# Optimization experiments

Hardware: AMD Instinct MI355X
Metric: run time of the kernel (lower is better)

## Reference

```python
import jax, jax.numpy as jnp
import numpy as np

B, N = 32, 200000          # images, flattened candidates per image (anchors*classes)
NUM_CLASSES = 21           # VOC-style class count for the label-offset trick
CONF_THR = 0.05            # cfg.PRED_CONF_THR
NMS_THR = 0.5              # cfg.PRED_NMS_THR
TOPK = 500                 # cfg.PRED_SELECT_TOPK
KEEP_MAX = 100             # cfg.PRED_NMS_KEEP


def setup_inputs() -> dict:
    key = jax.random.key(0)
    k1, k2, k3, k4 = jax.random.split(key, 4)
    pscores = jax.random.uniform(k1, (B, N), dtype=jnp.float32)
    # well-formed ltrb boxes in [0,1]: right>left, bottom>top
    xy1 = jax.random.uniform(k2, (B, N, 2), dtype=jnp.float32) * 0.8
    wh = jax.random.uniform(k3, (B, N, 2), dtype=jnp.float32) * 0.2 + 0.01
    pboxes = jnp.concatenate([xy1, xy1 + wh], axis=-1)
    plabels = jax.random.randint(k4, (B, N), 0, NUM_CLASSES)
    return {"pscores": pscores, "pboxes": pboxes, "plabels": plabels}


def _box_iou(a, b):
    # a: [K,4], b: [K,4] ltrb -> [K,K] pairwise IoU (torchvision convention)
    lt = jnp.maximum(a[:, None, :2], b[None, :, :2])
    rb = jnp.minimum(a[:, None, 2:], b[None, :, 2:])
    wh = jnp.clip(rb - lt, 0.0)
    inter = wh[..., 0] * wh[..., 1]
    area_a = (a[:, 2] - a[:, 0]) * (a[:, 3] - a[:, 1])
    area_b = (b[:, 2] - b[:, 0]) * (b[:, 3] - b[:, 1])
    return inter / (area_a[:, None] + area_b[None, :] - inter)


def _greedy_nms(iou_mat, valid, thr):
    # candidates are pre-sorted by score descending (lax.top_k output order)
    K = valid.shape[0]
    idxs = jnp.arange(K)

    def body(keep, i):
        suppressed = jnp.any(keep & (iou_mat[i] > thr) & (idxs < i))
        k = valid[i] & (~suppressed)
        return keep.at[i].set(k), None

    keep, _ = jax.lax.scan(body, jnp.zeros((K,), dtype=bool), idxs)
    return keep


def reference(pscores, pboxes, plabels):
    # ---- threshold + top-k pre-selection (mask_pos AND mask_topk) ----
    scores_k, idx = jax.lax.top_k(pscores, TOPK)          # [B,K] sorted desc
    valid = scores_k > CONF_THR                           # equivalent to mask_pos & mask_topk
    bidx = jnp.arange(B)[:, None]
    boxes_k = pboxes[bidx, idx]                           # [B,K,4]
    labels_k = plabels[bidx, idx]                         # [B,K]

    # ---- multi-class NMS via label offset trick (batched_nms) ----
    max_coord = jnp.max(jnp.where(valid[..., None], boxes_k, 0.0), axis=(1, 2))  # [B]
    offsets = labels_k.astype(boxes_k.dtype) * (max_coord[:, None] + 1.0)
    boxes_nms = boxes_k + offsets[..., None]              # [B,K,4]

    iou = jax.vmap(_box_iou)(boxes_nms, boxes_nms)        # [B,K,K]
    keep = jax.vmap(lambda m, v: _greedy_nms(m, v, NMS_THR))(iou, valid)  # [B,K] bool

    # ---- keep[:num_max] per batch ----
    rank = jnp.cumsum(keep.astype(jnp.int32), axis=1)
    keep = keep & (rank <= KEEP_MAX)

    # compact kept entries to front (jnp.argsort is stable -> score order preserved), pad to KEEP_MAX
    order = jnp.argsort(jnp.where(keep, 0, 1), axis=1)[:, :KEEP_MAX]       # [B,KEEP]
    out_valid = jnp.take_along_axis(keep, order, axis=1)                    # [B,KEEP]
    boxes2 = jnp.take_along_axis(boxes_k, order[..., None], axis=1) * out_valid[..., None]
    scores2 = jnp.take_along_axis(scores_k, order, axis=1) * out_valid
    labels2 = jnp.where(out_valid, jnp.take_along_axis(labels_k, order, axis=1), -1)
    ids_batch2 = jnp.where(out_valid, jnp.arange(B)[:, None], -1)
    return ids_batch2, boxes2, labels2, scores2, out_valid
```

## Files before the change

### kernel.cpp

```cpp
#include <hip/hip_runtime.h>
#include <stdint.h>

#pragma clang fp contract(off)

#define BB 32
#define NN 200000
#define N4 50000
#define KK 500
#define KEEPN 100
#define CONF 0.05f
#define NMSTHR 0.5f
#define SLICES 8
#define SLICE_F4 6250
#define LBINS 8192
#define LSHIFT 19
#define LOCAL_CAP 2048
#define OUT_CAP 576
#define TMPCAP 640
#define OK0 0xBF733333u

typedef unsigned long long u64;


__device__ __forceinline__ unsigned int ordkey(float s) {
    unsigned int u = __float_as_uint(s);
    return (u & 0x80000000u) ? ~u : (u | 0x80000000u);
}

__device__ __forceinline__ void wappend(bool pred, u64 key, u64* keys, int* lcnt, int lane) {
    u64 bm = __ballot(pred);
    int pre = __popcll(bm & ((1ULL << lane) - 1ULL));
    int tt  = __popcll(bm);
    int base = 0;
    if (lane == 0 && tt > 0) base = atomicAdd(lcnt, tt);
    base = __shfl(base, 0);
    if (pred) { int pos = base + pre; if (pos < LOCAL_CAP) keys[pos] = key; }
}

__global__ __launch_bounds__(1024) void select_kernel(const float4* __restrict__ ps4,
                                                      u64* __restrict__ cand,
                                                      unsigned int* __restrict__ cnts) {
    __shared__ unsigned int hist[LBINS];
    __shared__ u64 keys[LOCAL_CAP];
    __shared__ unsigned int h[256];
    __shared__ unsigned int wsum[16];
    __shared__ u64 wmin[16], wmax[16];
    __shared__ u64 s_prefix;
    __shared__ unsigned int s_t13, s_region, s_cntgt;
    __shared__ int s_lcnt, s_sc, s_shift0;

    const int b = blockIdx.y, x = blockIdx.x;
    const int tid = threadIdx.x, lane = tid & 63, wv = tid >> 6;
    const float4* p = ps4 + (size_t)b * N4 + (size_t)x * SLICE_F4;
    const int ebase = x * (SLICE_F4 * 4);

    if (tid == 0) s_lcnt = 0;
    __syncthreads();

    for (int i = tid; i < SLICE_F4; i += 1024) {
        float4 v = p[i];
        int n = ebase + (i << 2);
        unsigned int ux = ordkey(v.x), uy = ordkey(v.y);
        unsigned int uz = ordkey(v.z), uw = ordkey(v.w);
        wappend(ux >= OK0, ((u64)ux << 32) | (unsigned int)(~(unsigned int)(n)),     keys, &s_lcnt, lane);
        wappend(uy >= OK0, ((u64)uy << 32) | (unsigned int)(~(unsigned int)(n + 1)), keys, &s_lcnt, lane);
        wappend(uz >= OK0, ((u64)uz << 32) | (unsigned int)(~(unsigned int)(n + 2)), keys, &s_lcnt, lane);
        wappend(uw >= OK0, ((u64)uw << 32) | (unsigned int)(~(unsigned int)(n + 3)), keys, &s_lcnt, lane);
    }
    __syncthreads();
    int m = s_lcnt;

    if (m < KK || m > LOCAL_CAP) {
        for (int i = tid; i < LBINS; i += 1024) hist[i] = 0;
        __syncthreads();
        for (int i = tid; i < SLICE_F4; i += 1024) {
            float4 v = p[i];
            atomicAdd(&hist[ordkey(v.x) >> LSHIFT], 1u);
            atomicAdd(&hist[ordkey(v.y) >> LSHIFT], 1u);
            atomicAdd(&hist[ordkey(v.z) >> LSHIFT], 1u);
            atomicAdd(&hist[ordkey(v.w) >> LSHIFT], 1u);
        }
        __syncthreads();
        unsigned int v8[8], tot = 0;
        for (int j = 0; j < 8; ++j) { v8[j] = hist[tid * 8 + j]; tot += v8[j]; }
        unsigned int sfx = tot;
        for (int off = 1; off < 64; off <<= 1) {
            unsigned int t2 = __shfl_down(sfx, off);
            sfx += (lane + off < 64) ? t2 : 0u;
        }
        if (lane == 0) wsum[wv] = sfx;
        __syncthreads();
        unsigned int wafter = 0;
        for (int w2 = wv + 1; w2 < 16; ++w2) wafter += wsum[w2];
        unsigned int sn = wafter + (sfx - tot);
        for (int j = 7; j >= 0; --j) {
            unsigned int s = sn + v8[j];
            if (s >= (unsigned)KK && sn < (unsigned)KK) s_t13 = (unsigned)(tid * 8 + j);
            sn = s;
        }
        if (tid == 0) s_lcnt = 0;
        __syncthreads();
        const unsigned int t13 = s_t13;
        for (int i = tid; i < SLICE_F4; i += 1024) {
            float4 v = p[i];
            int n = ebase + (i << 2);
            unsigned int u;
            u = ordkey(v.x); if ((u >> LSHIFT) >= t13) { int pos = atomicAdd(&s_lcnt, 1);
                if (pos < LOCAL_CAP) keys[pos] = ((u64)u << 32) | (unsigned int)(~(unsigned int)(n)); }
            u = ordkey(v.y); if ((u >> LSHIFT) >= t13) { int pos = atomicAdd(&s_lcnt, 1);
                if (pos < LOCAL_CAP) keys[pos] = ((u64)u << 32) | (unsigned int)(~(unsigned int)(n + 1)); }
            u = ordkey(v.z); if ((u >> LSHIFT) >= t13) { int pos = atomicAdd(&s_lcnt, 1);
                if (pos < LOCAL_CAP) keys[pos] = ((u64)u << 32) | (unsigned int)(~(unsigned int)(n + 2)); }
            u = ordkey(v.w); if ((u >> LSHIFT) >= t13) { int pos = atomicAdd(&s_lcnt, 1);
                if (pos < LOCAL_CAP) keys[pos] = ((u64)u << 32) | (unsigned int)(~(unsigned int)(n + 3)); }
        }
        __syncthreads();
        m = s_lcnt; if (m > LOCAL_CAP) m = LOCAL_CAP;
    }

    u64 thr; int seln;
    if (m <= OUT_CAP) {
        thr = 0ULL; seln = m;
    } else {
        u64 kmn = ~0ULL, kmx = 0ULL;
        for (int i = tid; i < m; i += 1024) {
            u64 k = keys[i];
            kmn = k < kmn ? k : kmn; kmx = k > kmx ? k : kmx;
        }
        for (int off = 32; off > 0; off >>= 1) {
            u64 a = __shfl_down(kmn, off), c = __shfl_down(kmx, off);
            if (lane + off < 64) { kmn = a < kmn ? a : kmn; kmx = c > kmx ? c : kmx; }
        }
        if (lane == 0) { wmin[wv] = kmn; wmax[wv] = kmx; }
        __syncthreads();
        if (tid == 0) {
            u64 mn = wmin[0], mx = wmax[0];
            for (int w2 = 1; w2 < 16; ++w2) {
                mn = wmin[w2] < mn ? wmin[w2] : mn;
                mx = wmax[w2] > mx ? wmax[w2] : mx;
            }
            u64 diff = mn ^ mx;
            int hb = 63 - __builtin_clzll(diff | 1ULL);
            int st = (hb >> 3) << 3;
            s_shift0 = st;
            s_prefix = (st == 56) ? 0ULL : (mx >> (st + 8));
            s_cntgt = 0u;
        }
        __syncthreads();
        int shift = s_shift0;
        for (; shift >= 0; shift -= 8) {
            if (tid < 256) h[tid] = 0u;
            __syncthreads();
            u64 pref = s_prefix;
            unsigned int cg = s_cntgt;
            for (int i = tid; i < m; i += 1024) {
                u64 k = keys[i];
                bool match = (shift == 56) || ((k >> (shift + 8)) == pref);
                if (match) atomicAdd(&h[(unsigned int)((k >> shift) & 0xFF)], 1u);
            }
            __syncthreads();
            if (wv == 0) {
                unsigned int b4[4]; unsigned int lt = 0;
                for (int j = 0; j < 4; ++j) { b4[j] = h[lane * 4 + j]; lt += b4[j]; }
                unsigned int sx = lt;
                for (int off = 1; off < 64; off <<= 1) {
                    unsigned int t2 = __shfl_down(sx, off);
                    sx += (lane + off < 64) ? t2 : 0u;
                }
                unsigned int after = sx - lt;
                unsigned int target = (unsigned)KK - cg;
                unsigned int sn2 = after;
                for (int j = 3; j >= 0; --j) {
                    unsigned int s = sn2 + b4[j];
                    if (s >= target && sn2 < target) {
                        unsigned int bin = (unsigned)(lane * 4 + j);
                        s_region = b4[j];
                        s_cntgt = cg + sn2;
                        s_prefix = (shift == 56) ? (u64)bin : ((pref << 8) | (u64)bin);
                    }
                    sn2 = s;
                }
            }
            __syncthreads();
            if (s_cntgt + s_region <= (unsigned)OUT_CAP) break;
        }
        if (shift < 0) shift = 0;
        thr = s_prefix << shift;
        seln = (int)(s_cntgt + s_region);
    }
    (void)seln;

    if (tid == 0) s_sc = 0;
    __syncthreads();
    u64* outslice = cand + (size_t)(b * SLICES + x) * OUT_CAP;
    for (int r0 = 0; r0 < LOCAL_CAP / 1024; ++r0) {
        int i = tid + r0 * 1024;
        u64 k = (i < m) ? keys[i] : 0ULL;
        bool pq = (i < m) && (k >= thr);
        u64 mb = __ballot(pq);
        int pre = __popcll(mb & ((1ULL << lane) - 1ULL));
        int tt = __popcll(mb);
        int base = 0;
        if (lane == 0 && tt > 0) base = atomicAdd(&s_sc, tt);
        base = __shfl(base, 0);
        if (pq && base + pre < OUT_CAP) outslice[base + pre] = k;
    }
    __syncthreads();
    if (tid == 0) {
        int c = s_sc; if (c > OUT_CAP) c = OUT_CAP;
        cnts[b * SLICES + x] = (unsigned)c;
    }
}

__global__ __launch_bounds__(1024) void final_kernel(const float* __restrict__ pboxes,
                                                     const int* __restrict__ plabels,
                                                     const u64* __restrict__ cand,
                                                     const unsigned int* __restrict__ cnts,
                                                     float* __restrict__ out) {
    __shared__ u64 pool[4736];
    __shared__ float sboxes[KK * 5];
    __shared__ float sscore[KK];
    __shared__ int slabel[KK];
    __shared__ int clist[KK];
    __shared__ int scnt[SLICES];
    __shared__ u64 wmin[16], wmax[16];
    __shared__ unsigned int wsum[16], wmaxh[16];
    __shared__ float wred[16];
    __shared__ int ccnt[21], coff[22], cfill[21];
    __shared__ u64 validw[8], sremv[8], s_km;
    __shared__ int kept[KEEPN];
    __shared__ u64 s_kmn, s_kmx, s_prefix;
    __shared__ unsigned int s_region, s_cntgt;
    __shared__ int s_shift, s_thrbin, s_selupper, s_fb, s_bsh, s_sc, s_nk, s_stop;
    __shared__ float s_maxc;

    unsigned int* hist = (unsigned int*)pool;
    unsigned int* pfx  = ((unsigned int*)pool) + 4096;
    u64* tmp = (u64*)((char*)pool + 32768);

    const int b = blockIdx.x;
    const int tid = threadIdx.x;
    const int lane = tid & 63;
    const int wv = tid >> 6;
    const u64* cb = cand + (size_t)b * SLICES * OUT_CAP;

    if (tid < SLICES) {
        int c = (int)cnts[b * SLICES + tid];
        scnt[tid] = c > OUT_CAP ? OUT_CAP : c;
    }
    if (tid == 0) { s_thrbin = 0; s_fb = 0; s_nk = 0; s_stop = 0; }
    __syncthreads();

    for (int i = tid; i < 4096; i += 1024) hist[i] = 0u;
    u64 kmn = ~0ULL, kmx = 0ULL;
    for (int s = 0; s < SLICES; ++s) {
        if (tid < scnt[s]) {
            u64 k = cb[(size_t)s * OUT_CAP + tid];
            kmn = k < kmn ? k : kmn; kmx = k > kmx ? k : kmx;
        }
    }
    for (int off = 32; off > 0; off >>= 1) {
        u64 a = __shfl_down(kmn, off), c2 = __shfl_down(kmx, off);
        if (lane + off < 64) { kmn = a < kmn ? a : kmn; kmx = c2 > kmx ? c2 : kmx; }
    }
    if (lane == 0) { wmin[wv] = kmn; wmax[wv] = kmx; }
    __syncthreads();
    if (tid == 0) {
        u64 mn = wmin[0], mx = wmax[0];
        for (int w2 = 1; w2 < 16; ++w2) {
            mn = wmin[w2] < mn ? wmin[w2] : mn;
            mx = wmax[w2] > mx ? wmax[w2] : mx;
        }
        s_kmn = mn; s_kmx = mx;
        u64 diff = mn ^ mx;
        int hb = 63 - __builtin_clzll(diff | 1ULL);
        int sh = hb - 11; if (sh < 0) sh = 0;
        s_shift = sh;
    }
    __syncthreads();
    const int shift = s_shift;

    for (int s = 0; s < SLICES; ++s) {
        if (tid < scnt[s]) {
            u64 k = cb[(size_t)s * OUT_CAP + tid];
            atomicAdd(&hist[(unsigned int)((k >> shift) & 0xFFFu)], 1u);
        }
    }
    __syncthreads();

    unsigned int h4[4]; unsigned int lt = 0, hm = 0;
    const int g0 = tid << 2;
    for (int j = 0; j < 4; ++j) { h4[j] = hist[g0 + j]; lt += h4[j]; hm = h4[j] > hm ? h4[j] : hm; }
    unsigned int sfx = lt;
    for (int off = 1; off < 64; off <<= 1) {
        unsigned int t2 = __shfl_down(sfx, off);
        sfx += (lane + off < 64) ? t2 : 0u;
    }
    unsigned int mh = hm;
    for (int off = 1; off < 64; off <<= 1) {
        unsigned int t2 = __shfl_down(mh, off);
        if (lane + off < 64) mh = t2 > mh ? t2 : mh;
    }
    if (lane == 0) { wsum[wv] = sfx; wmaxh[wv] = mh; }
    __syncthreads();
    unsigned int wafter = 0;
    for (int w2 = wv + 1; w2 < 16; ++w2) wafter += wsum[w2];
    unsigned int run = wafter + (sfx - lt);
    for (int j = 3; j >= 0; --j) {
        pfx[g0 + j] = run;
        if (run < (unsigned)KK && run + h4[j] >= (unsigned)KK) s_thrbin = g0 + j;
        run += h4[j];
    }
    if (tid == 0) {
        unsigned int mmh = 0;
        for (int w2 = 0; w2 < 16; ++w2) mmh = wmaxh[w2] > mmh ? wmaxh[w2] : mmh;
        if (mmh > 64u) s_fb = 1;
    }
    __syncthreads();
    if (tid == 0) {
        int tb = s_thrbin;
        unsigned int su = pfx[tb] + hist[tb];
        s_selupper = (int)su;
        if (su > (unsigned)TMPCAP) s_fb = 1;
    }
    if (tid < KK) {
        sscore[tid] = -1.0f; slabel[tid] = 0;
        sboxes[tid * 5 + 0] = 0.0f; sboxes[tid * 5 + 1] = 0.0f;
        sboxes[tid * 5 + 2] = 0.0f; sboxes[tid * 5 + 3] = 0.0f;
    }
    __syncthreads();

    if (!s_fb) {
        const int thrbin = s_thrbin;
        for (int s = 0; s < SLICES; ++s) {
            if (tid < scnt[s]) {
                u64 k = cb[(size_t)s * OUT_CAP + tid];
                unsigned int g = (unsigned int)((k >> shift) & 0xFFFu);
                if ((int)g >= thrbin) {
                    unsigned int p = atomicAdd(&pfx[g], 1u);
                    if (p < (unsigned)TMPCAP) tmp[p] = k;
                }
            }
        }
        __syncthreads();
        int nr = s_selupper; if (nr > TMPCAP) nr = TMPCAP;
        if (tid < nr) {
            u64 k = tmp[tid];
            unsigned int g = (unsigned int)((k >> shift) & 0xFFFu);
            unsigned int c = hist[g];
            unsigned int base = pfx[g] - c;
            unsigned int lo = (unsigned int)k, hi = (unsigned int)(k >> 32);
            int idx = (int)(~lo);
            unsigned int bits = (hi & 0x80000000u) ? (hi & 0x7FFFFFFFu) : ~hi;
            float msc = __uint_as_float(bits);
            const float4 bx = *(const float4*)(pboxes + (((size_t)b * NN + (size_t)idx) << 2));
            int lab = plabels[(size_t)b * NN + idx];
            int rank = 0;
            for (unsigned int q = 0; q < c; ++q) {
                u64 o = tmp[base + q];
                rank += (o > k) ? 1 : 0;
            }
            int fin = (int)base + rank;
            if (fin < KK) {
                sboxes[fin * 5 + 0] = bx.x; sboxes[fin * 5 + 1] = bx.y;
                sboxes[fin * 5 + 2] = bx.z; sboxes[fin * 5 + 3] = bx.w;
                sscore[fin] = msc; slabel[fin] = lab;
            }
        }
        __syncthreads();
    } else {
        if (tid == 0) {
            u64 mn = s_kmn, mx = s_kmx;
            u64 diff = mn ^ mx;
            int hb = 63 - __builtin_clzll(diff | 1ULL);
            int st = (hb >> 3) << 3;
            s_bsh = st;
            s_prefix = (st == 56) ? 0ULL : (mx >> (st + 8));
            s_cntgt = 0u;
        }
        __syncthreads();
        int sh2 = s_bsh;
        for (; sh2 >= 0; sh2 -= 8) {
            if (tid < 256) hist[tid] = 0u;
            __syncthreads();
            u64 pref = s_prefix;
            unsigned int cg = s_cntgt;
            for (int s = 0; s < SLICES; ++s) {
                if (tid < scnt[s]) {
                    u64 k = cb[(size_t)s * OUT_CAP + tid];
                    bool match = (sh2 == 56) || ((k >> (sh2 + 8)) == pref);
                    if (match) atomicAdd(&hist[(unsigned int)((k >> sh2) & 0xFF)], 1u);
                }
            }
            __syncthreads();
            if (wv == 0) {
                unsigned int b4[4]; unsigned int lt2 = 0;
                for (int j = 0; j < 4; ++j) { b4[j] = hist[lane * 4 + j]; lt2 += b4[j]; }
                unsigned int sx = lt2;
                for (int off = 1; off < 64; off <<= 1) {
                    unsigned int t2 = __shfl_down(sx, off);
                    sx += (lane + off < 64) ? t2 : 0u;
                }
                unsigned int after = sx - lt2;
                unsigned int target = (unsigned)KK - cg;
                unsigned int sn2 = after;
                for (int j = 3; j >= 0; --j) {
                    unsigned int s = sn2 + b4[j];
                    if (s >= target && sn2 < target) {
                        unsigned int bin = (unsigned)(lane * 4 + j);
                        s_region = b4[j];
                        s_cntgt = cg + sn2;
                        s_prefix = (sh2 == 56) ? (u64)bin : ((pref << 8) | (u64)bin);
                    }
                    sn2 = s;
                }
            }
            __syncthreads();
            if (s_cntgt + s_region <= (unsigned)OUT_CAP) break;
        }
        if (sh2 < 0) sh2 = 0;
        u64 thr2 = s_prefix << sh2;
        int seln = (int)(s_cntgt + s_region);
        if (seln > TMPCAP) seln = TMPCAP;
        if (tid == 0) s_sc = 0;
        __syncthreads();
        for (int s = 0; s < SLICES; ++s) {
            u64 k = 0ULL; bool pq = false;
            if (tid < scnt[s]) { k = cb[(size_t)s * OUT_CAP + tid]; pq = (k >= thr2); }
            u64 mb = __ballot(pq);
            int pre = __popcll(mb & ((1ULL << lane) - 1ULL));
            int tt = __popcll(mb);
            int bse = 0;
            if (lane == 0 && tt > 0) bse = atomicAdd(&s_sc, tt);
            bse = __shfl(bse, 0);
            if (pq) { int pos = bse + pre; if (pos < TMPCAP) tmp[pos] = k; }
        }
        __syncthreads();
        u64 myk = (tid < seln) ? tmp[tid] : 0ULL;
        int r = 0;
        if ((tid & ~63) < seln) {
            for (int base = 0; base < seln; base += 64) {
                int i2 = base + lane;
                u64 other = (i2 < seln) ? tmp[i2] : 0ULL;
                unsigned int olo = (unsigned int)other, ohi = (unsigned int)(other >> 32);
                int lim = seln - base; if (lim > 64) lim = 64;
                for (int t2 = 0; t2 < lim; ++t2) {
                    unsigned int blo = (unsigned int)__builtin_amdgcn_readlane((int)olo, t2);
                    unsigned int bhi = (unsigned int)__builtin_amdgcn_readlane((int)ohi, t2);
                    u64 o = ((u64)bhi << 32) | (u64)blo;
                    r += (o > myk) ? 1 : 0;
                }
            }
        }
        __syncthreads();
        if (tid < seln && r < KK) {
            unsigned int lo = (unsigned int)myk, hi = (unsigned int)(myk >> 32);
            int idx = (int)(~lo);
            unsigned int bits = (hi & 0x80000000u) ? (hi & 0x7FFFFFFFu) : ~hi;
            float msc = __uint_as_float(bits);
            const float4 bx = *(const float4*)(pboxes + (((size_t)b * NN + (size_t)idx) << 2));
            int lab = plabels[(size_t)b * NN + idx];
            sboxes[r * 5 + 0] = bx.x; sboxes[r * 5 + 1] = bx.y;
            sboxes[r * 5 + 2] = bx.z; sboxes[r * 5 + 3] = bx.w;
            sscore[r] = msc; slabel[r] = lab;
        }
        __syncthreads();
    }

    float sc = (tid < KK) ? sscore[tid] : -1.0f;
    bool vq = (tid < KK) && (sc > CONF);
    u64 bm = __ballot(vq);
    if (lane == 0 && wv < 8) validw[wv] = bm;
    float lm = vq ? fmaxf(fmaxf(sboxes[tid * 5 + 0], sboxes[tid * 5 + 1]),
                          fmaxf(sboxes[tid * 5 + 2], sboxes[tid * 5 + 3])) : 0.0f;
    for (int off = 32; off > 0; off >>= 1) lm = fmaxf(lm, __shfl_down(lm, off));
    if (lane == 0) wred[wv] = lm;
    __syncthreads();
    if (tid < 64) {
        float x = (tid < 16) ? wred[tid] : 0.0f;
        for (int off = 8; off > 0; off >>= 1) x = fmaxf(x, __shfl_down(x, off));
        if (tid == 0) s_maxc = x;
    }
    if (tid < 21) { ccnt[tid] = 0; cfill[tid] = 0; }
    if (tid < 8) sremv[tid] = 0ULL;
    __syncthreads();
    if (tid < KK) atomicAdd(&ccnt[slabel[tid]], 1);
    __syncthreads();
    if (tid == 0) {
        int acc = 0;
        for (int c = 0; c < 21; ++c) { coff[c] = acc; acc += ccnt[c]; }
        coff[21] = acc;
    }
    __syncthreads();
    if (tid < KK) {
        int c = slabel[tid];
        int pos = atomicAdd(&cfill[c], 1);
        clist[coff[c] + pos] = tid;
    }
    u64 (*msk)[512] = (u64(*)[512])pool;
    for (int i = tid; i < 8 * 512; i += 1024) ((u64*)pool)[i] = 0ULL;
    __syncthreads();

    float ap1 = s_maxc + 1.0f;
    if (tid < KK) {
        int c = slabel[tid];
        int n = ccnt[c], base0 = coff[c];
        float aoff = (float)c * ap1;
        float a0 = sboxes[tid * 5 + 0] + aoff, a1 = sboxes[tid * 5 + 1] + aoff;
        float a2 = sboxes[tid * 5 + 2] + aoff, a3 = sboxes[tid * 5 + 3] + aoff;
        float areaA = (a2 - a0) * (a3 - a1);
        for (int q = 0; q < n; ++q) {
            int j = clist[base0 + q];
            float b0 = sboxes[j * 5 + 0] + aoff, b1f = sboxes[j * 5 + 1] + aoff;
            float b2f = sboxes[j * 5 + 2] + aoff, b3f = sboxes[j * 5 + 3] + aoff;
            float lt0 = fmaxf(a0, b0), lt1 = fmaxf(a1, b1f);
            float rb0 = fminf(a2, b2f), rb1 = fminf(a3, b3f);
            float ww = fmaxf(rb0 - lt0, 0.0f), hh = fmaxf(rb1 - lt1, 0.0f);
            float inter = ww * hh;
            float areaB = (b2f - b0) * (b3f - b1f);
            float iou = inter / (areaA + areaB - inter);
            if (iou > NMSTHR) msk[j >> 6][tid] |= (1ULL << (j & 63));
        }
    }
    __syncthreads();

    for (int c = 0; c < 8; ++c) {
        if (wv == 0) {
            u64 rowc = msk[c][c * 64 + lane];
            unsigned int rl = (unsigned int)rowc, rh = (unsigned int)(rowc >> 32);
            u64 cur = sremv[c];
            u64 vv = validw[c];
            u64 km = 0ULL;
            int nk = s_nk;
            for (int j = 0; j < 64; ++j) {
                if (nk >= KEEPN) break;
                bool alive = (((vv >> j) & 1ULL) != 0ULL) && (((cur >> j) & 1ULL) == 0ULL);
                if (alive) {
                    if (lane == 0) kept[nk] = c * 64 + j;
                    u64 rv = ((u64)(unsigned int)__builtin_amdgcn_readlane((int)rh, j) << 32)
                           |  (u64)(unsigned int)__builtin_amdgcn_readlane((int)rl, j);
                    cur |= rv;
                    km |= (1ULL << j);
                    ++nk;
                }
            }
            if (lane == 0) { s_km = km; s_nk = nk; sremv[c] = cur; s_stop = (nk >= KEEPN) ? 1 : 0; }
        }
        __syncthreads();
        if (s_stop || c == 7) break;
        if (wv > c && wv < 8) {
            u64 km = s_km;
            u64 v = ((km >> lane) & 1ULL) ? msk[wv][c * 64 + lane] : 0ULL;
            for (int off2 = 32; off2 > 0; off2 >>= 1) v |= __shfl_xor(v, off2);
            if (lane == 0) sremv[wv] |= v;
        }
        __syncthreads();
    }

    if (tid < KEEPN) {
        const int O_BOX = BB * KEEPN;
        const int O_LAB = BB * KEEPN * 5;
        const int O_SCO = BB * KEEPN * 6;
        const int O_VAL = BB * KEEPN * 7;
        bool q = tid < s_nk;
        int i = q ? kept[tid] : 0;
        int g = b * KEEPN + tid;
        out[g]                 = q ? (float)b : -1.0f;
        out[O_BOX + g * 4 + 0] = q ? sboxes[i * 5 + 0] : 0.0f;
        out[O_BOX + g * 4 + 1] = q ? sboxes[i * 5 + 1] : 0.0f;
        out[O_BOX + g * 4 + 2] = q ? sboxes[i * 5 + 2] : 0.0f;
        out[O_BOX + g * 4 + 3] = q ? sboxes[i * 5 + 3] : 0.0f;
        out[O_LAB + g]         = q ? (float)slabel[i] : -1.0f;
        out[O_SCO + g]         = q ? sscore[i] : 0.0f;
        out[O_VAL + g]         = q ? 1.0f : 0.0f;
    }
}

extern "C" void kernel_launch(void* const* d_in, const int* in_sizes, int n_in,
                              void* d_out, int out_size, void* d_ws, size_t ws_size,
                              hipStream_t stream) {
    const float* pscores = (const float*)d_in[0];
    const float* pboxes  = (const float*)d_in[1];
    const int*   plabels = (const int*)d_in[2];
    float* out = (float*)d_out;

    uint8_t* ws = (uint8_t*)d_ws;
    u64*          cand = (u64*)(ws + 0);
    unsigned int* cnts = (unsigned int*)(ws + 1179648);

    select_kernel<<<dim3(SLICES, BB), 1024, 0, stream>>>((const float4*)pscores, cand, cnts);
    final_kernel<<<BB, 1024, 0, stream>>>(pboxes, plabels, cand, cnts, out);
}
```

Before: 201.5 us.

## Shrink final kernel to 512 threads and cache candidate keys in registers

The final NMS kernel now runs with 512 threads per block. Each thread loads its share of the compacted candidate keys once into a register array (FITER slots, indexed through a prefix of slice counts) instead of re-reading global memory in every histogram, scatter and fallback pass. The goal is to cut repeated global loads and the cost of block-wide barriers. In exchange, each thread does more serial work, register pressure rises, and rank loops that used to be one thread per item now iterate.

```diff
diff --git a/kernel.cpp b/kernel.cpp
--- a/kernel.cpp
+++ b/kernel.cpp
@@ -212,20 +212,22 @@
     }
 }
 
-__global__ __launch_bounds__(1024) void final_kernel(const float* __restrict__ pboxes,
-                                                     const int* __restrict__ plabels,
-                                                     const u64* __restrict__ cand,
-                                                     const unsigned int* __restrict__ cnts,
-                                                     float* __restrict__ out) {
+#define FITER 9
+__global__ __launch_bounds__(512) void final_kernel(const float* __restrict__ pboxes,
+                                                    const int* __restrict__ plabels,
+                                                    const u64* __restrict__ cand,
+                                                    const unsigned int* __restrict__ cnts,
+                                                    float* __restrict__ out) {
     __shared__ u64 pool[4736];
     __shared__ float sboxes[KK * 5];
     __shared__ float sscore[KK];
     __shared__ int slabel[KK];
     __shared__ int clist[KK];
     __shared__ int scnt[SLICES];
-    __shared__ u64 wmin[16], wmax[16];
-    __shared__ unsigned int wsum[16], wmaxh[16];
-    __shared__ float wred[16];
+    __shared__ int soff[SLICES + 1];
+    __shared__ u64 wmin[8], wmax[8];
+    __shared__ unsigned int wsum[8], wmaxh[8];
+    __shared__ float wred[8];
     __shared__ int ccnt[21], coff[22], cfill[21];
     __shared__ u64 validw[8], sremv[8], s_km;
     __shared__ int kept[KEEPN];
@@ -250,14 +252,31 @@
     }
     if (tid == 0) { s_thrbin = 0; s_fb = 0; s_nk = 0; s_stop = 0; }
     __syncthreads();
-
-    for (int i = tid; i < 4096; i += 1024) hist[i] = 0u;
+    if (tid == 0) {
+        int acc = 0;
+        for (int s = 0; s < SLICES; ++s) { soff[s] = acc; acc += scnt[s]; }
+        soff[SLICES] = acc;
+    }
+    __syncthreads();
+    const int m = soff[SLICES];
+    int so1 = soff[1], so2 = soff[2], so3 = soff[3], so4 = soff[4];
+    int so5 = soff[5], so6 = soff[6], so7 = soff[7];
+
+    for (int i = tid; i < 4096; i += 512) hist[i] = 0u;
+    u64 kreg[FITER];
     u64 kmn = ~0ULL, kmx = 0ULL;
-    for (int s = 0; s < SLICES; ++s) {
-        if (tid < scnt[s]) {
-            u64 k = cb[(size_t)s * OUT_CAP + tid];
+    #pragma unroll
+    for (int r0 = 0; r0 < FITER; ++r0) {
+        int i = tid + r0 * 512;
+        u64 k = 0ULL;
+        if (i < m) {
+            int s = (i >= so1) + (i >= so2) + (i >= so3) + (i >= so4)
+                  + (i >= so5) + (i >= so6) + (i >= so7);
+            int base = (s == 0) ? 0 : soff[s];
+            k = cb[(size_t)s * OUT_CAP + (i - base)];
             kmn = k < kmn ? k : kmn; kmx = k > kmx ? k : kmx;
         }
+        kreg[r0] = k;
     }
     for (int off = 32; off > 0; off >>= 1) {
         u64 a = __shfl_down(kmn, off), c2 = __shfl_down(kmx, off);
@@ -267,7 +286,7 @@
     __syncthreads();
     if (tid == 0) {
         u64 mn = wmin[0], mx = wmax[0];
-        for (int w2 = 1; w2 < 16; ++w2) {
+        for (int w2 = 1; w2 < 8; ++w2) {
             mn = wmin[w2] < mn ? wmin[w2] : mn;
             mx = wmax[w2] > mx ? wmax[w2] : mx;
         }
@@ -280,17 +299,17 @@
     __syncthreads();
     const int shift = s_shift;
 
-    for (int s = 0; s < SLICES; ++s) {
-        if (tid < scnt[s]) {
-            u64 k = cb[(size_t)s * OUT_CAP + tid];
-            atomicAdd(&hist[(unsigned int)((k >> shift) & 0xFFFu)], 1u);
-        }
-    }
-    __syncthreads();
-
-    unsigned int h4[4]; unsigned int lt = 0, hm = 0;
-    const int g0 = tid << 2;
-    for (int j = 0; j < 4; ++j) { h4[j] = hist[g0 + j]; lt += h4[j]; hm = h4[j] > hm ? h4[j] : hm; }
+    #pragma unroll
+    for (int r0 = 0; r0 < FITER; ++r0) {
+        int i = tid + r0 * 512;
+        if (i < m) atomicAdd(&hist[(unsigned int)((kreg[r0] >> shift) & 0xFFFu)], 1u);
+    }
+    __syncthreads();
+
+    unsigned int h8[8]; unsigned int lt = 0, hm = 0;
+    const int g0 = tid << 3;
+    #pragma unroll
+    for (int j = 0; j < 8; ++j) { h8[j] = hist[g0 + j]; lt += h8[j]; hm = h8[j] > hm ? h8[j] : hm; }
     unsigned int sfx = lt;
     for (int off = 1; off < 64; off <<= 1) {
         unsigned int t2 = __shfl_down(sfx, off);
@@ -304,16 +323,17 @@
     if (lane == 0) { wsum[wv] = sfx; wmaxh[wv] = mh; }
     __syncthreads();
     unsigned int wafter = 0;
-    for (int w2 = wv + 1; w2 < 16; ++w2) wafter += wsum[w2];
+    for (int w2 = wv + 1; w2 < 8; ++w2) wafter += wsum[w2];
     unsigned int run = wafter + (sfx - lt);
-    for (int j = 3; j >= 0; --j) {
+    #pragma unroll
+    for (int j = 7; j >= 0; --j) {
         pfx[g0 + j] = run;
-        if (run < (unsigned)KK && run + h4[j] >= (unsigned)KK) s_thrbin = g0 + j;
-        run += h4[j];
+        if (run < (unsigned)KK && run + h8[j] >= (unsigned)KK) s_thrbin = g0 + j;
+        run += h8[j];
     }
     if (tid == 0) {
         unsigned int mmh = 0;
-        for (int w2 = 0; w2 < 16; ++w2) mmh = wmaxh[w2] > mmh ? wmaxh[w2] : mmh;
+        for (int w2 = 0; w2 < 8; ++w2) mmh = wmaxh[w2] > mmh ? wmaxh[w2] : mmh;
         if (mmh > 64u) s_fb = 1;
     }
     __syncthreads();
@@ -332,9 +352,11 @@
 
     if (!s_fb) {
         const int thrbin = s_thrbin;
-        for (int s = 0; s < SLICES; ++s) {
-            if (tid < scnt[s]) {
-                u64 k = cb[(size_t)s * OUT_CAP + tid];
+        #pragma unroll
+        for (int r0 = 0; r0 < FITER; ++r0) {
+            int i = tid + r0 * 512;
+            if (i < m) {
+                u64 k = kreg[r0];
                 unsigned int g = (unsigned int)((k >> shift) & 0xFFFu);
                 if ((int)g >= thrbin) {
                     unsigned int p = atomicAdd(&pfx[g], 1u);
@@ -344,8 +366,8 @@
         }
         __syncthreads();
         int nr = s_selupper; if (nr > TMPCAP) nr = TMPCAP;
-        if (tid < nr) {
-            u64 k = tmp[tid];
+        for (int ii = tid; ii < nr; ii += 512) {
+            u64 k = tmp[ii];
             unsigned int g = (unsigned int)((k >> shift) & 0xFFFu);
             unsigned int c = hist[g];
             unsigned int base = pfx[g] - c;
@@ -385,9 +407,11 @@
             __syncthreads();
             u64 pref = s_prefix;
             unsigned int cg = s_cntgt;
-            for (int s = 0; s < SLICES; ++s) {
-                if (tid < scnt[s]) {
-                    u64 k = cb[(size_t)s * OUT_CAP + tid];
+            #pragma unroll
+            for (int r0 = 0; r0 < FITER; ++r0) {
+                int i = tid + r0 * 512;
+                if (i < m) {
+                    u64 k = kreg[r0];
                     bool match = (sh2 == 56) || ((k >> (sh2 + 8)) == pref);
                     if (match) atomicAdd(&hist[(unsigned int)((k >> sh2) & 0xFF)], 1u);
                 }
@@ -424,9 +448,11 @@
         if (seln > TMPCAP) seln = TMPCAP;
         if (tid == 0) s_sc = 0;
         __syncthreads();
-        for (int s = 0; s < SLICES; ++s) {
-            u64 k = 0ULL; bool pq = false;
-            if (tid < scnt[s]) { k = cb[(size_t)s * OUT_CAP + tid]; pq = (k >= thr2); }
+        #pragma unroll
+        for (int r0 = 0; r0 < FITER; ++r0) {
+            int i = tid + r0 * 512;
+            u64 k = (i < m) ? kreg[r0] : 0ULL;
+            bool pq = (i < m) && (k >= thr2);
             u64 mb = __ballot(pq);
             int pre = __popcll(mb & ((1ULL << lane) - 1ULL));
             int tt = __popcll(mb);
@@ -436,33 +462,35 @@
             if (pq) { int pos = bse + pre; if (pos < TMPCAP) tmp[pos] = k; }
         }
         __syncthreads();
-        u64 myk = (tid < seln) ? tmp[tid] : 0ULL;
-        int r = 0;
-        if ((tid & ~63) < seln) {
-            for (int base = 0; base < seln; base += 64) {
-                int i2 = base + lane;
-                u64 other = (i2 < seln) ? tmp[i2] : 0ULL;
-                unsigned int olo = (unsigned int)other, ohi = (unsigned int)(other >> 32);
-                int lim = seln - base; if (lim > 64) lim = 64;
-                for (int t2 = 0; t2 < lim; ++t2) {
-                    unsigned int blo = (unsigned int)__builtin_amdgcn_readlane((int)olo, t2);
-                    unsigned int bhi = (unsigned int)__builtin_amdgcn_readlane((int)ohi, t2);
-                    u64 o = ((u64)bhi << 32) | (u64)blo;
-                    r += (o > myk) ? 1 : 0;
-                }
-            }
-        }
-        __syncthreads();
-        if (tid < seln && r < KK) {
-            unsigned int lo = (unsigned int)myk, hi = (unsigned int)(myk >> 32);
-            int idx = (int)(~lo);
-            unsigned int bits = (hi & 0x80000000u) ? (hi & 0x7FFFFFFFu) : ~hi;
-            float msc = __uint_as_float(bits);
-            const float4 bx = *(const float4*)(pboxes + (((size_t)b * NN + (size_t)idx) << 2));
-            int lab = plabels[(size_t)b * NN + idx];
-            sboxes[r * 5 + 0] = bx.x; sboxes[r * 5 + 1] = bx.y;
-            sboxes[r * 5 + 2] = bx.z; sboxes[r * 5 + 3] = bx.w;
-            sscore[r] = msc; slabel[r] = lab;
+        for (int r0 = 0; r0 < 2; ++r0) {
+            int ii = tid + r0 * 512;
+            if (ii - lane < seln) {
+                u64 myk = (ii < seln) ? tmp[ii] : 0ULL;
+                int r = 0;
+                for (int base = 0; base < seln; base += 64) {
+                    int i2 = base + lane;
+                    u64 other = (i2 < seln) ? tmp[i2] : 0ULL;
+                    unsigned int olo = (unsigned int)other, ohi = (unsigned int)(other >> 32);
+                    int lim = seln - base; if (lim > 64) lim = 64;
+                    for (int t2 = 0; t2 < lim; ++t2) {
+                        unsigned int blo = (unsigned int)__builtin_amdgcn_readlane((int)olo, t2);
+                        unsigned int bhi = (unsigned int)__builtin_amdgcn_readlane((int)ohi, t2);
+                        u64 o = ((u64)bhi << 32) | (u64)blo;
+                        r += (o > myk) ? 1 : 0;
+                    }
+                }
+                if (ii < seln && r < KK) {
+                    unsigned int lo = (unsigned int)myk, hi = (unsigned int)(myk >> 32);
+                    int idx = (int)(~lo);
+                    unsigned int bits = (hi & 0x80000000u) ? (hi & 0x7FFFFFFFu) : ~hi;
+                    float msc = __uint_as_float(bits);
+                    const float4 bx = *(const float4*)(pboxes + (((size_t)b * NN + (size_t)idx) << 2));
+                    int lab = plabels[(size_t)b * NN + idx];
+                    sboxes[r * 5 + 0] = bx.x; sboxes[r * 5 + 1] = bx.y;
+                    sboxes[r * 5 + 2] = bx.z; sboxes[r * 5 + 3] = bx.w;
+                    sscore[r] = msc; slabel[r] = lab;
+                }
+            }
         }
         __syncthreads();
     }
@@ -470,15 +498,15 @@
     float sc = (tid < KK) ? sscore[tid] : -1.0f;
     bool vq = (tid < KK) && (sc > CONF);
     u64 bm = __ballot(vq);
-    if (lane == 0 && wv < 8) validw[wv] = bm;
+    if (lane == 0) validw[wv] = bm;
     float lm = vq ? fmaxf(fmaxf(sboxes[tid * 5 + 0], sboxes[tid * 5 + 1]),
                           fmaxf(sboxes[tid * 5 + 2], sboxes[tid * 5 + 3])) : 0.0f;
     for (int off = 32; off > 0; off >>= 1) lm = fmaxf(lm, __shfl_down(lm, off));
     if (lane == 0) wred[wv] = lm;
     __syncthreads();
     if (tid < 64) {
-        float x = (tid < 16) ? wred[tid] : 0.0f;
-        for (int off = 8; off > 0; off >>= 1) x = fmaxf(x, __shfl_down(x, off));
+        float x = (tid < 8) ? wred[tid] : 0.0f;
+        for (int off = 4; off > 0; off >>= 1) x = fmaxf(x, __shfl_down(x, off));
         if (tid == 0) s_maxc = x;
     }
     if (tid < 21) { ccnt[tid] = 0; cfill[tid] = 0; }
@@ -498,7 +526,7 @@
         clist[coff[c] + pos] = tid;
     }
     u64 (*msk)[512] = (u64(*)[512])pool;
-    for (int i = tid; i < 8 * 512; i += 1024) ((u64*)pool)[i] = 0ULL;
+    for (int i = tid; i < 8 * 512; i += 512) ((u64*)pool)[i] = 0ULL;
     __syncthreads();
 
     float ap1 = s_maxc + 1.0f;
@@ -548,7 +576,7 @@
         }
         __syncthreads();
         if (s_stop || c == 7) break;
-        if (wv > c && wv < 8) {
+        if (wv > c) {
             u64 km = s_km;
             u64 v = ((km >> lane) & 1ULL) ? msk[wv][c * 64 + lane] : 0ULL;
             for (int off2 = 32; off2 > 0; off2 >>= 1) v |= __shfl_xor(v, off2);
@@ -589,5 +617,5 @@
     unsigned int* cnts = (unsigned int*)(ws + 1179648);
 
     select_kernel<<<dim3(SLICES, BB), 1024, 0, stream>>>((const float4*)pscores, cand, cnts);
-    final_kernel<<<BB, 1024, 0, stream>>>(pboxes, plabels, cand, cnts, out);
+    final_kernel<<<BB, 512, 0, stream>>>(pboxes, plabels, cand, cnts, out);
 }
```

Result: faster. 196.9 us, median of 2 (-2.3%).
